# Kernel optimization log

Measured on AMD Instinct MI355X. Metric: run time of the kernel, lower is better.

## Reference

```python
import jax, jax.numpy as jnp
import numpy as np

KW = 3  # kernel_width


def setup_inputs() -> dict:
    key = jax.random.key(0)
    k0, k1, k2, k3, k4 = jax.random.split(key, 5)
    L, B, C, Q, V = 2048, 64, 512, 512, 512
    q = jax.random.normal(k0, (B, Q), dtype=jnp.float32)
    k = jax.random.normal(k1, (L, B, C), dtype=jnp.float32)
    v = jax.random.normal(k2, (L, B, V), dtype=jnp.float32)
    k_mask = jax.random.randint(k3, (L, B), 0, 2, dtype=jnp.int32)
    k_mask = k_mask.at[0].set(1)  # ensure at least one valid position per column
    # q_to_kernel Linear params: weight [k_size*KW, q_size], bias [k_size*KW]
    W = jax.random.normal(k4, (C * KW, Q), dtype=jnp.float32) / np.float32(np.sqrt(Q))
    b = jnp.zeros((C * KW,), dtype=jnp.float32)
    return {"q": q, "k": k, "v": v, "k_mask": k_mask, "W": W, "b": b}


def reference(q, k, v, k_mask, W, b):
    L, B, C = k.shape
    # dynamically generated per-sample grouped-conv kernels: [B, C, KW]
    kernel = (q @ W.T + b).reshape(B, C, KW)
    pad = (KW - 1) // 2
    k_pad = jnp.pad(k, ((pad, pad), (0, 0), (0, 0)))  # [L+2*pad, B, C]
    # sliding-window score: a_ij[t,b] = sum_{c,w} k[t+w-pad,b,c] * kernel[b,c,w]
    a_ij = jnp.zeros((L, B), dtype=k.dtype)
    for w in range(KW):  # tiny static loop over kernel taps
        a_ij = a_ij + jnp.einsum('lbc,bc->lb', k_pad[w:w + L], kernel[:, :, w])
    # masked softmax over kv_len (dim 0)
    maskb = k_mask.astype(bool)
    neg = jnp.finfo(a_ij.dtype).min
    e_ij = jax.nn.softmax(jnp.where(maskb, a_ij, neg), axis=0) * k_mask.astype(a_ij.dtype)
    # weighted sum of v: [B, V]
    attend = jnp.einsum('lb,lbv->bv', e_ij, v)
    return a_ij, e_ij, attend
```

## Files before the change

### kernel.cpp

```cpp
#include <hip/hip_runtime.h>
#include <float.h>
#include <math.h>

#define Ln 2048
#define Bn 64
#define Cn 512
#define Qn 512
#define Vn 512
#define NO 1536

#define DROW 2064
#define DPAD 8

#define OFF_KERN 0
#define OFF_DPL  98304
#define OFF_ABT  (OFF_DPL + 396288)
#define OFF_ET   (OFF_ABT + 131072)
#define OFF_CST  (OFF_ET + 131072)
#define OFF_SCR  (OFF_CST + 1024)

typedef float f4 __attribute__((ext_vector_type(4)));
typedef float f2 __attribute__((ext_vector_type(2)));

__global__ __launch_bounds__(256) void k1_gemm(const float* __restrict__ q,
                                               const float* __restrict__ W,
                                               float* __restrict__ gpart) {
    __shared__ __align__(16) float qs[64][68];
    __shared__ __align__(16) float wsm[64][68];
    const int o0 = blockIdx.x * 64;
    const int k0 = blockIdx.y * 128;
    const int tid = threadIdx.x;
    const int ty = tid >> 4, tx = tid & 15;

    f4 accv[4][4];
#pragma unroll
    for (int i = 0; i < 4; ++i)
#pragma unroll
        for (int j = 0; j < 4; ++j) accv[i][j] = (f4)0.f;

    for (int kc = 0; kc < 128; kc += 64) {
#pragma unroll
        for (int r = 0; r < 4; ++r) {
            int idx = tid + r * 256;
            int row = idx >> 4;
            int c4 = (idx & 15) << 2;
            float4 vq = *(const float4*)&q[row * Qn + k0 + kc + c4];
            qs[row][c4 + 0] = vq.x; qs[row][c4 + 1] = vq.y;
            qs[row][c4 + 2] = vq.z; qs[row][c4 + 3] = vq.w;
            float4 vw = *(const float4*)&W[(o0 + row) * Qn + k0 + kc + c4];
            wsm[row][c4 + 0] = vw.x; wsm[row][c4 + 1] = vw.y;
            wsm[row][c4 + 2] = vw.z; wsm[row][c4 + 3] = vw.w;
        }
        __syncthreads();
#pragma unroll
        for (int kk4 = 0; kk4 < 16; ++kk4) {
            f4 qf[4], wf[4];
#pragma unroll
            for (int i = 0; i < 4; ++i) qf[i] = *(const f4*)&qs[ty * 4 + i][kk4 * 4];
#pragma unroll
            for (int j = 0; j < 4; ++j) wf[j] = *(const f4*)&wsm[tx * 4 + j][kk4 * 4];
#pragma unroll
            for (int i = 0; i < 4; ++i)
#pragma unroll
                for (int j = 0; j < 4; ++j) accv[i][j] += qf[i] * wf[j];
        }
        __syncthreads();
    }
#pragma unroll
    for (int i = 0; i < 4; ++i) {
        float4 w4;
        f4 p;
        p = accv[i][0]; w4.x = (p.x + p.y) + (p.z + p.w);
        p = accv[i][1]; w4.y = (p.x + p.y) + (p.z + p.w);
        p = accv[i][2]; w4.z = (p.x + p.y) + (p.z + p.w);
        p = accv[i][3]; w4.w = (p.x + p.y) + (p.z + p.w);
        *(float4*)&gpart[(blockIdx.y * 64 + ty * 4 + i) * NO + o0 + tx * 4] = w4;
    }
}

__global__ __launch_bounds__(256) void k1b_reduce(const float* __restrict__ gpart,
                                                  const float* __restrict__ bias,
                                                  float* __restrict__ kern) {
    int idx = blockIdx.x * 256 + threadIdx.x;
    if (idx >= 3 * Bn * Cn) return;
    int w = idx / (Bn * Cn);
    int rem = idx - w * (Bn * Cn);
    int b = rem >> 9;
    int c = rem & 511;
    int o = c * 3 + w;
    float s = bias[o];
#pragma unroll
    for (int ks = 0; ks < 4; ++ks) s += gpart[(ks * Bn + b) * NO + o];
    kern[idx] = s;
}

__global__ __launch_bounds__(256) void k2_dots(const float* __restrict__ kin,
                                               const float* __restrict__ kern,
                                               float* __restrict__ dplP) {
    const int wid = (blockIdx.x << 2) + (threadIdx.x >> 6);
    const int lane = threadIdx.x & 63;
    const int b = wid & 63;
    const int t0 = (wid >> 6) << 3;

    f4 kwA[3], kwB[3];
#pragma unroll
    for (int w = 0; w < 3; ++w) {
        const f4* p = (const f4*)(kern + (w * Bn + b) * Cn);
        kwA[w] = p[lane];
        kwB[w] = p[64 + lane];
    }
#pragma unroll
    for (int ti = 0; ti < 8; ++ti) {
        const int t = t0 + ti;
        const f4* kr = (const f4*)(kin + ((size_t)t * Bn + b) * Cn);
        f4 a = __builtin_nontemporal_load(kr + lane);
        f4 c = __builtin_nontemporal_load(kr + 64 + lane);
        float acc0 = a.x * kwA[0].x + a.y * kwA[0].y + a.z * kwA[0].z + a.w * kwA[0].w
                   + c.x * kwB[0].x + c.y * kwB[0].y + c.z * kwB[0].z + c.w * kwB[0].w;
        float acc1 = a.x * kwA[1].x + a.y * kwA[1].y + a.z * kwA[1].z + a.w * kwA[1].w
                   + c.x * kwB[1].x + c.y * kwB[1].y + c.z * kwB[1].z + c.w * kwB[1].w;
        float acc2 = a.x * kwA[2].x + a.y * kwA[2].y + a.z * kwA[2].z + a.w * kwA[2].w
                   + c.x * kwB[2].x + c.y * kwB[2].y + c.z * kwB[2].z + c.w * kwB[2].w;
#pragma unroll
        for (int off = 32; off; off >>= 1) {
            acc0 += __shfl_xor(acc0, off);
            acc1 += __shfl_xor(acc1, off);
            acc2 += __shfl_xor(acc2, off);
        }
        if (lane == 0) {
            dplP[(0 * Bn + b) * DROW + DPAD + t] = acc0;
            dplP[(1 * Bn + b) * DROW + DPAD + t] = acc1;
            dplP[(2 * Bn + b) * DROW + DPAD + t] = acc2;
        }
    }
}

__global__ __launch_bounds__(256) void kA_stats(const float* __restrict__ dplP,
                                                const int* __restrict__ kmask,
                                                float* __restrict__ aBT,
                                                float* __restrict__ cstat) {
    const int b = blockIdx.x & 63;
    const int c = blockIdx.x >> 6;
    const int tid = threadIdx.x;
    const int t = c * 256 + tid;
    __shared__ float red[4];

    const float* d0 = dplP + (0 * Bn + b) * DROW + DPAD;
    const float* d1 = dplP + (1 * Bn + b) * DROW + DPAD;
    const float* d2 = dplP + (2 * Bn + b) * DROW + DPAD;
    const float x0 = d0[t - 1];
    const float x2 = d2[t + 1];
    const float a = d1[t] + (t > 0 ? x0 : 0.f) + (t < Ln - 1 ? x2 : 0.f);
    const int m = kmask[t * Bn + b];
    aBT[b * Ln + t] = a;

    float lmax = m ? a : -FLT_MAX;
#pragma unroll
    for (int off = 32; off; off >>= 1) lmax = fmaxf(lmax, __shfl_xor(lmax, off));
    if ((tid & 63) == 0) red[tid >> 6] = lmax;
    __syncthreads();
    const float mxc = fmaxf(fmaxf(red[0], red[1]), fmaxf(red[2], red[3]));
    __syncthreads();
    float lsum = m ? __expf(a - mxc) : 0.f;
#pragma unroll
    for (int off = 32; off; off >>= 1) lsum += __shfl_xor(lsum, off);
    if ((tid & 63) == 0) red[tid >> 6] = lsum;
    __syncthreads();
    if (tid == 0) {
        cstat[(b * 8 + c) * 2 + 0] = mxc;
        cstat[(b * 8 + c) * 2 + 1] = red[0] + red[1] + red[2] + red[3];
    }
}

__global__ __launch_bounds__(256) void kB_pv(const float* __restrict__ aBT,
                                             const int* __restrict__ kmask,
                                             const float* __restrict__ cstat,
                                             const float* __restrict__ v,
                                             float* __restrict__ eT,
                                             float* __restrict__ vpart) {
    const int b = blockIdx.x & 63;
    const int c = blockIdx.x >> 6;
    const int tid = threadIdx.x;
    const int t = c * 256 + tid;

    const float* cs = cstat + b * 16;
    float mx = -FLT_MAX;
#pragma unroll
    for (int j = 0; j < 8; ++j)
        if (cs[2 * j + 1] > 0.f) mx = fmaxf(mx, cs[2 * j]);
    float sum = 0.f;
#pragma unroll
    for (int j = 0; j < 8; ++j)
        if (cs[2 * j + 1] > 0.f) sum += cs[2 * j + 1] * __expf(cs[2 * j] - mx);
    const float inv = 1.f / sum;

    const float a = aBT[b * Ln + t];
    const int m = kmask[t * Bn + b];
    const float e = m ? __expf(a - mx) * inv : 0.f;
    eT[b * Ln + t] = e;

    __shared__ float es[256];
    __shared__ unsigned long long bm[4];
    es[tid] = e;
    unsigned long long bal = __ballot(e != 0.f);
    if ((tid & 63) == 0) bm[tid >> 6] = bal;
    __syncthreads();

    f2 a0 = (f2)0.f, a1 = (f2)0.f;
#pragma unroll
    for (int w = 0; w < 4; ++w) {
        unsigned long long mm = bm[w];
        while (mm) {
            int bit = __ffsll(mm) - 1;
            mm &= mm - 1;
            int tt = w * 64 + bit;
            float ee = es[tt];
            const f2* vrow = (const f2*)(v + (((size_t)(c * 256 + tt) * Bn + b) << 9));
            f2 vv = __builtin_nontemporal_load(vrow + tid);
            if (mm) {
                int bit2 = __ffsll(mm) - 1;
                mm &= mm - 1;
                int tt2 = w * 64 + bit2;
                float ee2 = es[tt2];
                const f2* vrow2 = (const f2*)(v + (((size_t)(c * 256 + tt2) * Bn + b) << 9));
                f2 vv2 = __builtin_nontemporal_load(vrow2 + tid);
                a0 += ee * vv;
                a1 += ee2 * vv2;
            } else {
                a0 += ee * vv;
            }
        }
    }
    f2 s = a0 + a1;
    *(f2*)&vpart[((c * Bn + b) << 9) + tid * 2] = s;
}

__global__ __launch_bounds__(256) void kC_fin(const float* __restrict__ aBT,
                                              const float* __restrict__ eT,
                                              const float* __restrict__ vpart,
                                              float* __restrict__ out_a,
                                              float* __restrict__ out_e,
                                              float* __restrict__ out_att) {
    const int bid = blockIdx.x;
    const int tid = threadIdx.x;
    __shared__ __align__(16) float lsa[64][17];
    __shared__ __align__(16) float lse[64][17];

    if (bid < 128) {
        const int t0 = bid * 16;
        const int rb = tid >> 2;
        const int ri = tid & 3;
        f4 av = *(const f4*)&aBT[rb * Ln + t0 + ri * 4];
        f4 ev = *(const f4*)&eT[rb * Ln + t0 + ri * 4];
#pragma unroll
        for (int j = 0; j < 4; ++j) {
            lsa[rb][ri * 4 + j] = av[j];
            lse[rb][ri * 4 + j] = ev[j];
        }
        __syncthreads();
        const int tt = tid >> 4;
        const int c4 = tid & 15;
        f4 oa, oe;
#pragma unroll
        for (int j = 0; j < 4; ++j) {
            oa[j] = lsa[c4 * 4 + j][tt];
            oe[j] = lse[c4 * 4 + j][tt];
        }
        *(f4*)&out_a[(t0 + tt) * Bn + c4 * 4] = oa;
        *(f4*)&out_e[(t0 + tt) * Bn + c4 * 4] = oe;
    } else {
        const int idx = (bid - 128) * 256 + tid;
        float s = 0.f;
#pragma unroll
        for (int cc = 0; cc < 8; ++cc) s += vpart[cc * (Bn * Vn) + idx];
        out_att[idx] = s;
    }
}

extern "C" void kernel_launch(void* const* d_in, const int* in_sizes, int n_in,
                              void* d_out, int out_size, void* d_ws, size_t ws_size,
                              hipStream_t stream) {
    const float* q = (const float*)d_in[0];
    const float* k = (const float*)d_in[1];
    const float* v = (const float*)d_in[2];
    const int* kmask = (const int*)d_in[3];
    const float* W = (const float*)d_in[4];
    const float* bias = (const float*)d_in[5];

    float* out = (float*)d_out;
    float* out_a = out;
    float* out_e = out + Ln * Bn;
    float* out_att = out + 2 * Ln * Bn;

    float* ws = (float*)d_ws;
    float* kern = ws + OFF_KERN;
    float* dplP = ws + OFF_DPL;
    float* aBT = ws + OFF_ABT;
    float* eT = ws + OFF_ET;
    float* cstat = ws + OFF_CST;
    float* scr = ws + OFF_SCR;

    k1_gemm<<<dim3(24, 4), 256, 0, stream>>>(q, W, scr);
    k1b_reduce<<<(3 * Bn * Cn + 255) / 256, 256, 0, stream>>>(scr, bias, kern);
    k2_dots<<<4096, 256, 0, stream>>>(k, kern, dplP);
    kA_stats<<<512, 256, 0, stream>>>(dplP, kmask, aBT, cstat);
    kB_pv<<<512, 256, 0, stream>>>(aBT, kmask, cstat, v, eT, scr);
    kC_fin<<<256, 256, 0, stream>>>(aBT, eT, scr, out_a, out_e, out_att);
}
```

Before: 84.26 us.

## Fuse tap dot products with score assembly and chunk softmax stats

Merges the per-tap dot-product kernel with the score/statistics kernel. Each block computes 32 time rows for one batch plus halo rows recomputed from k, keeps the three tap sums in shared memory, and then writes the assembled scores and per-32-row max/sum stats. This removes one launch and the global round-trip through the padded dot buffer. In exchange it re-reads two halo rows of k per block (about 6% extra k traffic), and the next kernel now merges 64 chunk stats instead of 8.

```diff
diff --git a/kernel.cpp b/kernel.cpp
--- a/kernel.cpp
+++ b/kernel.cpp
@@ -9,15 +9,11 @@
 #define Vn 512
 #define NO 1536
 
-#define DROW 2064
-#define DPAD 8
-
 #define OFF_KERN 0
-#define OFF_DPL  98304
-#define OFF_ABT  (OFF_DPL + 396288)
+#define OFF_ABT  98304
 #define OFF_ET   (OFF_ABT + 131072)
 #define OFF_CST  (OFF_ET + 131072)
-#define OFF_SCR  (OFF_CST + 1024)
+#define OFF_SCR  (OFF_CST + 8192)
 
 typedef float f4 __attribute__((ext_vector_type(4)));
 typedef float f2 __attribute__((ext_vector_type(2)));
@@ -94,13 +90,20 @@
     kern[idx] = s;
 }
 
-__global__ __launch_bounds__(256) void k2_dots(const float* __restrict__ kin,
-                                               const float* __restrict__ kern,
-                                               float* __restrict__ dplP) {
-    const int wid = (blockIdx.x << 2) + (threadIdx.x >> 6);
+__global__ __launch_bounds__(256) void k2a(const float* __restrict__ kin,
+                                           const float* __restrict__ kern,
+                                           const int* __restrict__ kmask,
+                                           float* __restrict__ aBT,
+                                           float* __restrict__ cstat) {
+    __shared__ float d0s[34], d1s[34], d2s[34];
+    const int b = blockIdx.x & 63;
+    const int tc = blockIdx.x >> 6;
+    const int base = tc << 5;
+    const int wv = threadIdx.x >> 6;
     const int lane = threadIdx.x & 63;
-    const int b = wid & 63;
-    const int t0 = (wid >> 6) << 3;
+
+    if (threadIdx.x == 0 && base == 0) d0s[0] = 0.f;
+    if (threadIdx.x == 1 && base + 32 >= Ln) d2s[33] = 0.f;
 
     f4 kwA[3], kwB[3];
 #pragma unroll
@@ -109,10 +112,11 @@
         kwA[w] = p[lane];
         kwB[w] = p[64 + lane];
     }
+
 #pragma unroll
     for (int ti = 0; ti < 8; ++ti) {
-        const int t = t0 + ti;
-        const f4* kr = (const f4*)(kin + ((size_t)t * Bn + b) * Cn);
+        const int r = base + (wv << 3) + ti;
+        const f4* kr = (const f4*)(kin + ((size_t)r * Bn + b) * Cn);
         f4 a = __builtin_nontemporal_load(kr + lane);
         f4 c = __builtin_nontemporal_load(kr + 64 + lane);
         float acc0 = a.x * kwA[0].x + a.y * kwA[0].y + a.z * kwA[0].z + a.w * kwA[0].w
@@ -128,47 +132,51 @@
             acc2 += __shfl_xor(acc2, off);
         }
         if (lane == 0) {
-            dplP[(0 * Bn + b) * DROW + DPAD + t] = acc0;
-            dplP[(1 * Bn + b) * DROW + DPAD + t] = acc1;
-            dplP[(2 * Bn + b) * DROW + DPAD + t] = acc2;
-        }
-    }
-}
-
-__global__ __launch_bounds__(256) void kA_stats(const float* __restrict__ dplP,
-                                                const int* __restrict__ kmask,
-                                                float* __restrict__ aBT,
-                                                float* __restrict__ cstat) {
-    const int b = blockIdx.x & 63;
-    const int c = blockIdx.x >> 6;
-    const int tid = threadIdx.x;
-    const int t = c * 256 + tid;
-    __shared__ float red[4];
-
-    const float* d0 = dplP + (0 * Bn + b) * DROW + DPAD;
-    const float* d1 = dplP + (1 * Bn + b) * DROW + DPAD;
-    const float* d2 = dplP + (2 * Bn + b) * DROW + DPAD;
-    const float x0 = d0[t - 1];
-    const float x2 = d2[t + 1];
-    const float a = d1[t] + (t > 0 ? x0 : 0.f) + (t < Ln - 1 ? x2 : 0.f);
-    const int m = kmask[t * Bn + b];
-    aBT[b * Ln + t] = a;
-
-    float lmax = m ? a : -FLT_MAX;
-#pragma unroll
-    for (int off = 32; off; off >>= 1) lmax = fmaxf(lmax, __shfl_xor(lmax, off));
-    if ((tid & 63) == 0) red[tid >> 6] = lmax;
+            const int idx = (wv << 3) + ti + 1;
+            d0s[idx] = acc0;
+            d1s[idx] = acc1;
+            d2s[idx] = acc2;
+        }
+    }
+    if (wv == 0 && base > 0) {
+        const f4* kr = (const f4*)(kin + ((size_t)(base - 1) * Bn + b) * Cn);
+        f4 a = __builtin_nontemporal_load(kr + lane);
+        f4 c = __builtin_nontemporal_load(kr + 64 + lane);
+        float acc0 = a.x * kwA[0].x + a.y * kwA[0].y + a.z * kwA[0].z + a.w * kwA[0].w
+                   + c.x * kwB[0].x + c.y * kwB[0].y + c.z * kwB[0].z + c.w * kwB[0].w;
+#pragma unroll
+        for (int off = 32; off; off >>= 1) acc0 += __shfl_xor(acc0, off);
+        if (lane == 0) d0s[0] = acc0;
+    }
+    if (wv == 3 && base + 32 < Ln) {
+        const f4* kr = (const f4*)(kin + ((size_t)(base + 32) * Bn + b) * Cn);
+        f4 a = __builtin_nontemporal_load(kr + lane);
+        f4 c = __builtin_nontemporal_load(kr + 64 + lane);
+        float acc2 = a.x * kwA[2].x + a.y * kwA[2].y + a.z * kwA[2].z + a.w * kwA[2].w
+                   + c.x * kwB[2].x + c.y * kwB[2].y + c.z * kwB[2].z + c.w * kwB[2].w;
+#pragma unroll
+        for (int off = 32; off; off >>= 1) acc2 += __shfl_xor(acc2, off);
+        if (lane == 0) d2s[33] = acc2;
+    }
     __syncthreads();
-    const float mxc = fmaxf(fmaxf(red[0], red[1]), fmaxf(red[2], red[3]));
-    __syncthreads();
-    float lsum = m ? __expf(a - mxc) : 0.f;
-#pragma unroll
-    for (int off = 32; off; off >>= 1) lsum += __shfl_xor(lsum, off);
-    if ((tid & 63) == 0) red[tid >> 6] = lsum;
-    __syncthreads();
-    if (tid == 0) {
-        cstat[(b * 8 + c) * 2 + 0] = mxc;
-        cstat[(b * 8 + c) * 2 + 1] = red[0] + red[1] + red[2] + red[3];
+
+    if (threadIdx.x < 32) {
+        const int i = threadIdx.x;
+        const int t = base + i;
+        const float a = d1s[i + 1] + d0s[i] + d2s[i + 2];
+        const int m = kmask[t * Bn + b];
+        aBT[b * Ln + t] = a;
+
+        float mxc = m ? a : -FLT_MAX;
+#pragma unroll
+        for (int off = 16; off; off >>= 1) mxc = fmaxf(mxc, __shfl_xor(mxc, off, 32));
+        float lsum = m ? __expf(a - mxc) : 0.f;
+#pragma unroll
+        for (int off = 16; off; off >>= 1) lsum += __shfl_xor(lsum, off, 32);
+        if (i == 0) {
+            cstat[(b * 64 + tc) * 2 + 0] = mxc;
+            cstat[(b * 64 + tc) * 2 + 1] = lsum;
+        }
     }
 }
 
@@ -183,14 +191,14 @@
     const int tid = threadIdx.x;
     const int t = c * 256 + tid;
 
-    const float* cs = cstat + b * 16;
+    const float* cs = cstat + b * 128;
     float mx = -FLT_MAX;
-#pragma unroll
-    for (int j = 0; j < 8; ++j)
+#pragma unroll 8
+    for (int j = 0; j < 64; ++j)
         if (cs[2 * j + 1] > 0.f) mx = fmaxf(mx, cs[2 * j]);
     float sum = 0.f;
-#pragma unroll
-    for (int j = 0; j < 8; ++j)
+#pragma unroll 8
+    for (int j = 0; j < 64; ++j)
         if (cs[2 * j + 1] > 0.f) sum += cs[2 * j + 1] * __expf(cs[2 * j] - mx);
     const float inv = 1.f / sum;
 
@@ -294,7 +302,6 @@
 
     float* ws = (float*)d_ws;
     float* kern = ws + OFF_KERN;
-    float* dplP = ws + OFF_DPL;
     float* aBT = ws + OFF_ABT;
     float* eT = ws + OFF_ET;
     float* cstat = ws + OFF_CST;
@@ -302,8 +309,7 @@
 
     k1_gemm<<<dim3(24, 4), 256, 0, stream>>>(q, W, scr);
     k1b_reduce<<<(3 * Bn * Cn + 255) / 256, 256, 0, stream>>>(scr, bias, kern);
-    k2_dots<<<4096, 256, 0, stream>>>(k, kern, dplP);
-    kA_stats<<<512, 256, 0, stream>>>(dplP, kmask, aBT, cstat);
+    k2a<<<4096, 256, 0, stream>>>(k, kern, kmask, aBT, cstat);
     kB_pv<<<512, 256, 0, stream>>>(aBT, kmask, cstat, v, eT, scr);
     kC_fin<<<256, 256, 0, stream>>>(aBT, eT, scr, out_a, out_e, out_att);
 }
```

Result: slower. 89.22 us (+5.9%).

## Fuse softmax stats and PV into one kernel with inter-block spin barrier

Applied to the files above, without the earlier changes.

Merges the per-chunk softmax statistics kernel and the weighted-V accumulation kernel into a single kernel. Each of the 4 blocks per batch column handles 512 positions, publishes its partial max and sum, then spins on a per-batch atomic counter until all 4 partials are in before normalizing and accumulating V. This removes a launch and the re-read of scores and mask. In exchange the grid shrinks to 256 blocks, which lowers parallelism on the V reads, and correctness depends on all blocks of a batch being co-resident for the spin wait.

```diff
diff --git a/kernel.cpp b/kernel.cpp
--- a/kernel.cpp
+++ b/kernel.cpp
@@ -17,7 +17,8 @@
 #define OFF_ABT  (OFF_DPL + 396288)
 #define OFF_ET   (OFF_ABT + 131072)
 #define OFF_CST  (OFF_ET + 131072)
-#define OFF_SCR  (OFF_CST + 1024)
+#define OFF_CNT  (OFF_CST + 1024)
+#define OFF_SCR  (OFF_CNT + 64)
 
 typedef float f4 __attribute__((ext_vector_type(4)));
 typedef float f2 __attribute__((ext_vector_type(2)));
@@ -80,7 +81,9 @@
 
 __global__ __launch_bounds__(256) void k1b_reduce(const float* __restrict__ gpart,
                                                   const float* __restrict__ bias,
-                                                  float* __restrict__ kern) {
+                                                  float* __restrict__ kern,
+                                                  int* __restrict__ cnt) {
+    if (blockIdx.x == 0 && threadIdx.x < Bn) cnt[threadIdx.x] = 0;
     int idx = blockIdx.x * 256 + threadIdx.x;
     if (idx >= 3 * Bn * Cn) return;
     int w = idx / (Bn * Cn);
@@ -135,104 +138,114 @@
     }
 }
 
-__global__ __launch_bounds__(256) void kA_stats(const float* __restrict__ dplP,
-                                                const int* __restrict__ kmask,
-                                                float* __restrict__ aBT,
-                                                float* __restrict__ cstat) {
+__global__ __launch_bounds__(256, 2) void kAB(const float* __restrict__ dplP,
+                                              const int* __restrict__ kmask,
+                                              const float* __restrict__ v,
+                                              float* __restrict__ aBT,
+                                              float* __restrict__ eT,
+                                              float* __restrict__ cstat,
+                                              int* __restrict__ cnt,
+                                              float* __restrict__ vpart) {
     const int b = blockIdx.x & 63;
-    const int c = blockIdx.x >> 6;
+    const int h = blockIdx.x >> 6;
     const int tid = threadIdx.x;
-    const int t = c * 256 + tid;
+    const int t1 = h * 512 + tid;
+    const int t2 = t1 + 256;
+
     __shared__ float red[4];
+    __shared__ float sh[2];
+    __shared__ float es[512];
+    __shared__ unsigned long long bm[8];
 
     const float* d0 = dplP + (0 * Bn + b) * DROW + DPAD;
     const float* d1 = dplP + (1 * Bn + b) * DROW + DPAD;
     const float* d2 = dplP + (2 * Bn + b) * DROW + DPAD;
-    const float x0 = d0[t - 1];
-    const float x2 = d2[t + 1];
-    const float a = d1[t] + (t > 0 ? x0 : 0.f) + (t < Ln - 1 ? x2 : 0.f);
-    const int m = kmask[t * Bn + b];
-    aBT[b * Ln + t] = a;
-
-    float lmax = m ? a : -FLT_MAX;
+    const float x01 = d0[t1 - 1], x21 = d2[t1 + 1];
+    const float a1 = d1[t1] + (t1 > 0 ? x01 : 0.f) + (t1 < Ln - 1 ? x21 : 0.f);
+    const float x02 = d0[t2 - 1], x22 = d2[t2 + 1];
+    const float a2 = d1[t2] + (t2 > 0 ? x02 : 0.f) + (t2 < Ln - 1 ? x22 : 0.f);
+    const int m1 = kmask[t1 * Bn + b];
+    const int m2 = kmask[t2 * Bn + b];
+    aBT[b * Ln + t1] = a1;
+    aBT[b * Ln + t2] = a2;
+
+    float lmax = fmaxf(m1 ? a1 : -FLT_MAX, m2 ? a2 : -FLT_MAX);
 #pragma unroll
     for (int off = 32; off; off >>= 1) lmax = fmaxf(lmax, __shfl_xor(lmax, off));
     if ((tid & 63) == 0) red[tid >> 6] = lmax;
     __syncthreads();
     const float mxc = fmaxf(fmaxf(red[0], red[1]), fmaxf(red[2], red[3]));
     __syncthreads();
-    float lsum = m ? __expf(a - mxc) : 0.f;
+    float lsum = (m1 ? __expf(a1 - mxc) : 0.f) + (m2 ? __expf(a2 - mxc) : 0.f);
 #pragma unroll
     for (int off = 32; off; off >>= 1) lsum += __shfl_xor(lsum, off);
     if ((tid & 63) == 0) red[tid >> 6] = lsum;
     __syncthreads();
+
     if (tid == 0) {
-        cstat[(b * 8 + c) * 2 + 0] = mxc;
-        cstat[(b * 8 + c) * 2 + 1] = red[0] + red[1] + red[2] + red[3];
-    }
-}
-
-__global__ __launch_bounds__(256) void kB_pv(const float* __restrict__ aBT,
-                                             const int* __restrict__ kmask,
-                                             const float* __restrict__ cstat,
-                                             const float* __restrict__ v,
-                                             float* __restrict__ eT,
-                                             float* __restrict__ vpart) {
-    const int b = blockIdx.x & 63;
-    const int c = blockIdx.x >> 6;
-    const int tid = threadIdx.x;
-    const int t = c * 256 + tid;
-
-    const float* cs = cstat + b * 16;
-    float mx = -FLT_MAX;
-#pragma unroll
-    for (int j = 0; j < 8; ++j)
-        if (cs[2 * j + 1] > 0.f) mx = fmaxf(mx, cs[2 * j]);
-    float sum = 0.f;
-#pragma unroll
-    for (int j = 0; j < 8; ++j)
-        if (cs[2 * j + 1] > 0.f) sum += cs[2 * j + 1] * __expf(cs[2 * j] - mx);
-    const float inv = 1.f / sum;
-
-    const float a = aBT[b * Ln + t];
-    const int m = kmask[t * Bn + b];
-    const float e = m ? __expf(a - mx) * inv : 0.f;
-    eT[b * Ln + t] = e;
-
-    __shared__ float es[256];
-    __shared__ unsigned long long bm[4];
-    es[tid] = e;
-    unsigned long long bal = __ballot(e != 0.f);
-    if ((tid & 63) == 0) bm[tid >> 6] = bal;
-    __syncthreads();
-
-    f2 a0 = (f2)0.f, a1 = (f2)0.f;
-#pragma unroll
-    for (int w = 0; w < 4; ++w) {
+        cstat[b * 16 + h * 2 + 0] = mxc;
+        cstat[b * 16 + h * 2 + 1] = red[0] + red[1] + red[2] + red[3];
+        __threadfence();
+        atomicAdd(&cnt[b], 1);
+        while (atomicAdd(&cnt[b], 0) < 4) {}
+        __threadfence();
+        const float* cs = cstat + b * 16;
+        float mx = -FLT_MAX;
+#pragma unroll
+        for (int j = 0; j < 4; ++j)
+            if (cs[2 * j + 1] > 0.f) mx = fmaxf(mx, cs[2 * j]);
+        float sum = 0.f;
+#pragma unroll
+        for (int j = 0; j < 4; ++j)
+            if (cs[2 * j + 1] > 0.f) sum += cs[2 * j + 1] * __expf(cs[2 * j] - mx);
+        sh[0] = mx;
+        sh[1] = 1.f / sum;
+    }
+    __syncthreads();
+    const float mx = sh[0];
+    const float inv = sh[1];
+
+    const float e1 = m1 ? __expf(a1 - mx) * inv : 0.f;
+    const float e2 = m2 ? __expf(a2 - mx) * inv : 0.f;
+    eT[b * Ln + t1] = e1;
+    eT[b * Ln + t2] = e2;
+    es[tid] = e1;
+    es[256 + tid] = e2;
+    unsigned long long bal1 = __ballot(e1 != 0.f);
+    unsigned long long bal2 = __ballot(e2 != 0.f);
+    if ((tid & 63) == 0) {
+        bm[tid >> 6] = bal1;
+        bm[4 + (tid >> 6)] = bal2;
+    }
+    __syncthreads();
+
+    f2 a0 = (f2)0.f, a1v = (f2)0.f;
+#pragma unroll
+    for (int w = 0; w < 8; ++w) {
         unsigned long long mm = bm[w];
         while (mm) {
             int bit = __ffsll(mm) - 1;
             mm &= mm - 1;
             int tt = w * 64 + bit;
             float ee = es[tt];
-            const f2* vrow = (const f2*)(v + (((size_t)(c * 256 + tt) * Bn + b) << 9));
+            const f2* vrow = (const f2*)(v + (((size_t)(h * 512 + tt) * Bn + b) << 9));
             f2 vv = __builtin_nontemporal_load(vrow + tid);
             if (mm) {
                 int bit2 = __ffsll(mm) - 1;
                 mm &= mm - 1;
                 int tt2 = w * 64 + bit2;
                 float ee2 = es[tt2];
-                const f2* vrow2 = (const f2*)(v + (((size_t)(c * 256 + tt2) * Bn + b) << 9));
+                const f2* vrow2 = (const f2*)(v + (((size_t)(h * 512 + tt2) * Bn + b) << 9));
                 f2 vv2 = __builtin_nontemporal_load(vrow2 + tid);
                 a0 += ee * vv;
-                a1 += ee2 * vv2;
+                a1v += ee2 * vv2;
             } else {
                 a0 += ee * vv;
             }
         }
     }
-    f2 s = a0 + a1;
-    *(f2*)&vpart[((c * Bn + b) << 9) + tid * 2] = s;
+    f2 s = a0 + a1v;
+    *(f2*)&vpart[((h * Bn + b) << 9) + tid * 2] = s;
 }
 
 __global__ __launch_bounds__(256) void kC_fin(const float* __restrict__ aBT,
@@ -272,7 +285,7 @@
         const int idx = (bid - 128) * 256 + tid;
         float s = 0.f;
 #pragma unroll
-        for (int cc = 0; cc < 8; ++cc) s += vpart[cc * (Bn * Vn) + idx];
+        for (int cc = 0; cc < 4; ++cc) s += vpart[cc * (Bn * Vn) + idx];
         out_att[idx] = s;
     }
 }
@@ -298,12 +311,12 @@
     float* aBT = ws + OFF_ABT;
     float* eT = ws + OFF_ET;
     float* cstat = ws + OFF_CST;
+    int* cnt = (int*)(ws + OFF_CNT);
     float* scr = ws + OFF_SCR;
 
     k1_gemm<<<dim3(24, 4), 256, 0, stream>>>(q, W, scr);
-    k1b_reduce<<<(3 * Bn * Cn + 255) / 256, 256, 0, stream>>>(scr, bias, kern);
+    k1b_reduce<<<(3 * Bn * Cn + 255) / 256, 256, 0, stream>>>(scr, bias, kern, cnt);
     k2_dots<<<4096, 256, 0, stream>>>(k, kern, dplP);
-    kA_stats<<<512, 256, 0, stream>>>(dplP, kmask, aBT, cstat);
-    kB_pv<<<512, 256, 0, stream>>>(aBT, kmask, cstat, v, eT, scr);
+    kAB<<<256, 256, 0, stream>>>(dplP, kmask, v, aBT, eT, cstat, cnt, scr);
     kC_fin<<<256, 256, 0, stream>>>(aBT, eT, scr, out_a, out_e, out_att);
 }
```

New measurement: 102.1 us. 21.1% more time.

## Write a/e outputs directly, pre-mask scores, compact nonzero list for PV loop

Applied to the files above, without the earlier changes.

kA_stats now writes a_ij straight into the [L,B] output and also stores a pre-masked copy of the scores (-1e30 where masked), so kB_pv no longer has to read k_mask. kB_pv writes e_ij directly to the output and builds a compacted shared-memory list of nonzero time steps. The V accumulation then runs over that list, unrolled four-wide with independent accumulators, instead of serial ballot bit-scanning. The transpose stage in kC_fin is dropped, which removes an intermediate buffer and its round trip; the cost is strided scalar stores into the [L,B] outputs.

```diff
diff --git a/kernel.cpp b/kernel.cpp
--- a/kernel.cpp
+++ b/kernel.cpp
@@ -15,8 +15,7 @@
 #define OFF_KERN 0
 #define OFF_DPL  98304
 #define OFF_ABT  (OFF_DPL + 396288)
-#define OFF_ET   (OFF_ABT + 131072)
-#define OFF_CST  (OFF_ET + 131072)
+#define OFF_CST  (OFF_ABT + 131072)
 #define OFF_SCR  (OFF_CST + 1024)
 
 typedef float f4 __attribute__((ext_vector_type(4)));
@@ -137,7 +136,8 @@
 
 __global__ __launch_bounds__(256) void kA_stats(const float* __restrict__ dplP,
                                                 const int* __restrict__ kmask,
-                                                float* __restrict__ aBT,
+                                                float* __restrict__ out_a,
+                                                float* __restrict__ aBTm,
                                                 float* __restrict__ cstat) {
     const int b = blockIdx.x & 63;
     const int c = blockIdx.x >> 6;
@@ -152,7 +152,8 @@
     const float x2 = d2[t + 1];
     const float a = d1[t] + (t > 0 ? x0 : 0.f) + (t < Ln - 1 ? x2 : 0.f);
     const int m = kmask[t * Bn + b];
-    aBT[b * Ln + t] = a;
+    out_a[t * Bn + b] = a;
+    aBTm[b * Ln + t] = m ? a : -1e30f;
 
     float lmax = m ? a : -FLT_MAX;
 #pragma unroll
@@ -172,11 +173,10 @@
     }
 }
 
-__global__ __launch_bounds__(256) void kB_pv(const float* __restrict__ aBT,
-                                             const int* __restrict__ kmask,
+__global__ __launch_bounds__(256) void kB_pv(const float* __restrict__ aBTm,
                                              const float* __restrict__ cstat,
                                              const float* __restrict__ v,
-                                             float* __restrict__ eT,
+                                             float* __restrict__ out_e,
                                              float* __restrict__ vpart) {
     const int b = blockIdx.x & 63;
     const int c = blockIdx.x >> 6;
@@ -194,87 +194,60 @@
         if (cs[2 * j + 1] > 0.f) sum += cs[2 * j + 1] * __expf(cs[2 * j] - mx);
     const float inv = 1.f / sum;
 
-    const float a = aBT[b * Ln + t];
-    const int m = kmask[t * Bn + b];
-    const float e = m ? __expf(a - mx) * inv : 0.f;
-    eT[b * Ln + t] = e;
+    const float am = aBTm[b * Ln + t];
+    const float e = __expf(am - mx) * inv;
+    out_e[t * Bn + b] = e;
 
     __shared__ float es[256];
     __shared__ unsigned long long bm[4];
+    __shared__ int lst[256];
     es[tid] = e;
-    unsigned long long bal = __ballot(e != 0.f);
+    const unsigned long long bal = __ballot(e != 0.f);
     if ((tid & 63) == 0) bm[tid >> 6] = bal;
     __syncthreads();
 
-    f2 a0 = (f2)0.f, a1 = (f2)0.f;
-#pragma unroll
-    for (int w = 0; w < 4; ++w) {
-        unsigned long long mm = bm[w];
-        while (mm) {
-            int bit = __ffsll(mm) - 1;
-            mm &= mm - 1;
-            int tt = w * 64 + bit;
-            float ee = es[tt];
-            const f2* vrow = (const f2*)(v + (((size_t)(c * 256 + tt) * Bn + b) << 9));
-            f2 vv = __builtin_nontemporal_load(vrow + tid);
-            if (mm) {
-                int bit2 = __ffsll(mm) - 1;
-                mm &= mm - 1;
-                int tt2 = w * 64 + bit2;
-                float ee2 = es[tt2];
-                const f2* vrow2 = (const f2*)(v + (((size_t)(c * 256 + tt2) * Bn + b) << 9));
-                f2 vv2 = __builtin_nontemporal_load(vrow2 + tid);
-                a0 += ee * vv;
-                a1 += ee2 * vv2;
-            } else {
-                a0 += ee * vv;
-            }
-        }
-    }
-    f2 s = a0 + a1;
+    const int wv = tid >> 6;
+    const int lane = tid & 63;
+    int off = 0;
+#pragma unroll
+    for (int w = 0; w < 4; ++w)
+        if (w < wv) off += __popcll(bm[w]);
+    if (e != 0.f) {
+        int rank = __popcll(bal & ((1ull << lane) - 1ull));
+        lst[off + rank] = tid;
+    }
+    const int n = __popcll(bm[0]) + __popcll(bm[1]) + __popcll(bm[2]) + __popcll(bm[3]);
+    __syncthreads();
+
+    f2 a0 = (f2)0.f, a1 = (f2)0.f, a2 = (f2)0.f, a3 = (f2)0.f;
+    int i = 0;
+    for (; i + 4 <= n; i += 4) {
+        const int t0 = lst[i], t1 = lst[i + 1], t2 = lst[i + 2], t3 = lst[i + 3];
+        const f2 v0 = __builtin_nontemporal_load((const f2*)(v + (((size_t)(c * 256 + t0) * Bn + b) << 9)) + tid);
+        const f2 v1 = __builtin_nontemporal_load((const f2*)(v + (((size_t)(c * 256 + t1) * Bn + b) << 9)) + tid);
+        const f2 v2 = __builtin_nontemporal_load((const f2*)(v + (((size_t)(c * 256 + t2) * Bn + b) << 9)) + tid);
+        const f2 v3 = __builtin_nontemporal_load((const f2*)(v + (((size_t)(c * 256 + t3) * Bn + b) << 9)) + tid);
+        a0 += es[t0] * v0;
+        a1 += es[t1] * v1;
+        a2 += es[t2] * v2;
+        a3 += es[t3] * v3;
+    }
+    for (; i < n; ++i) {
+        const int tt = lst[i];
+        const f2 vv = __builtin_nontemporal_load((const f2*)(v + (((size_t)(c * 256 + tt) * Bn + b) << 9)) + tid);
+        a0 += es[tt] * vv;
+    }
+    const f2 s = (a0 + a1) + (a2 + a3);
     *(f2*)&vpart[((c * Bn + b) << 9) + tid * 2] = s;
 }
 
-__global__ __launch_bounds__(256) void kC_fin(const float* __restrict__ aBT,
-                                              const float* __restrict__ eT,
-                                              const float* __restrict__ vpart,
-                                              float* __restrict__ out_a,
-                                              float* __restrict__ out_e,
+__global__ __launch_bounds__(256) void kC_fin(const float* __restrict__ vpart,
                                               float* __restrict__ out_att) {
-    const int bid = blockIdx.x;
-    const int tid = threadIdx.x;
-    __shared__ __align__(16) float lsa[64][17];
-    __shared__ __align__(16) float lse[64][17];
-
-    if (bid < 128) {
-        const int t0 = bid * 16;
-        const int rb = tid >> 2;
-        const int ri = tid & 3;
-        f4 av = *(const f4*)&aBT[rb * Ln + t0 + ri * 4];
-        f4 ev = *(const f4*)&eT[rb * Ln + t0 + ri * 4];
-#pragma unroll
-        for (int j = 0; j < 4; ++j) {
-            lsa[rb][ri * 4 + j] = av[j];
-            lse[rb][ri * 4 + j] = ev[j];
-        }
-        __syncthreads();
-        const int tt = tid >> 4;
-        const int c4 = tid & 15;
-        f4 oa, oe;
-#pragma unroll
-        for (int j = 0; j < 4; ++j) {
-            oa[j] = lsa[c4 * 4 + j][tt];
-            oe[j] = lse[c4 * 4 + j][tt];
-        }
-        *(f4*)&out_a[(t0 + tt) * Bn + c4 * 4] = oa;
-        *(f4*)&out_e[(t0 + tt) * Bn + c4 * 4] = oe;
-    } else {
-        const int idx = (bid - 128) * 256 + tid;
-        float s = 0.f;
-#pragma unroll
-        for (int cc = 0; cc < 8; ++cc) s += vpart[cc * (Bn * Vn) + idx];
-        out_att[idx] = s;
-    }
+    const int idx = blockIdx.x * 256 + threadIdx.x;
+    float s = 0.f;
+#pragma unroll
+    for (int cc = 0; cc < 8; ++cc) s += vpart[cc * (Bn * Vn) + idx];
+    out_att[idx] = s;
 }
 
 extern "C" void kernel_launch(void* const* d_in, const int* in_sizes, int n_in,
@@ -295,15 +268,14 @@
     float* ws = (float*)d_ws;
     float* kern = ws + OFF_KERN;
     float* dplP = ws + OFF_DPL;
-    float* aBT = ws + OFF_ABT;
-    float* eT = ws + OFF_ET;
+    float* aBTm = ws + OFF_ABT;
     float* cstat = ws + OFF_CST;
     float* scr = ws + OFF_SCR;
 
     k1_gemm<<<dim3(24, 4), 256, 0, stream>>>(q, W, scr);
     k1b_reduce<<<(3 * Bn * Cn + 255) / 256, 256, 0, stream>>>(scr, bias, kern);
     k2_dots<<<4096, 256, 0, stream>>>(k, kern, dplP);
-    kA_stats<<<512, 256, 0, stream>>>(dplP, kmask, aBT, cstat);
-    kB_pv<<<512, 256, 0, stream>>>(aBT, kmask, cstat, v, eT, scr);
-    kC_fin<<<256, 256, 0, stream>>>(aBT, eT, scr, out_a, out_e, out_att);
-}
+    kA_stats<<<512, 256, 0, stream>>>(dplP, kmask, out_a, aBTm, cstat);
+    kB_pv<<<512, 256, 0, stream>>>(aBTm, cstat, v, out_e, scr);
+    kC_fin<<<128, 256, 0, stream>>>(scr, out_att);
+}
```

After: 78.91 us. 1.07x faster.
